# Optimization experiments

Measured on AMD Instinct MI355X. Metric: run time of the kernel, lower is better.

Reference implementation:

```python
import jax, jax.numpy as jnp
import numpy as np

_HIST_BINS = 64
TOP_K_FRAC = 0.125
HIST_THRESHOLD = 2048


def setup_inputs() -> dict:
    key = jax.random.key(0)
    B, S = 256, 131072
    importance = jax.random.normal(key, (B, S), dtype=jnp.float32)
    return {"importance": importance, "S": S}


def reference(importance, S):
    # importance: [B, S] float32; S: python int
    K = max(1, int(TOP_K_FRAC * S))
    if S > HIST_THRESHOLD:
        # Histogram bookkeeping path (computed but unused by the original module;
        # reproduced here for faithfulness to the source's memory traffic).
        imin = jnp.min(importance, axis=-1, keepdims=True)  # [B,1]
        imax = jnp.max(importance, axis=-1, keepdims=True)  # [B,1]
        rng = jnp.clip(imax - imin, 1e-8, None)
        bin_idx = ((importance - imin) / rng * (_HIST_BINS - 1)).astype(jnp.int32)
        bin_idx = jnp.clip(bin_idx, 0, _HIST_BINS - 1)  # [B,S]
        B = importance.shape[0]
        rows = jnp.arange(B)[:, None]  # [B,1] broadcast against [B,S]
        hist = jnp.zeros((B, _HIST_BINS), dtype=jnp.int32).at[rows, bin_idx].add(1)
        del hist  # dead value, exactly as in the torch source
    _, top_idx = jax.lax.top_k(importance, K)  # [B,K] indices into last dim
    return (top_idx, K)
```

## Files before the change

kernel.cpp:

```cpp
#include <hip/hip_runtime.h>
#include <stdint.h>


#define S_LEN   131072
#define K_SEL   16384
#define NBINS   8192
#define LOWBITS 19
#define IDXMASK 0x1FFFFu
#define CAND_CAP 20480
#define SORT_CAP 4096
#define DIRECT_MAX 256
#define WL_PER_ROW 2048
#define D_GRID  2048
#define HCAP 256
#define LCAP 512
#define NWAVE 16
#define PC_WAVE 1664
#define NITER (S_LEN / 4 / 1024)
#define BU0 ((0x3F800000u ^ 0x80000000u) >> LOWBITS)

__device__ __forceinline__ unsigned int ordered_u32(float f) {
  unsigned int x = __float_as_uint(f);
  unsigned int mask = (unsigned int)((int)x >> 31) | 0x80000000u;
  return x ^ mask;
}

__global__ __launch_bounds__(1024)
void select_kernel(const float* __restrict__ in,
                   unsigned long long* __restrict__ pairs,
                   unsigned long long* __restrict__ cand,
                   uint4* __restrict__ wl, unsigned int* __restrict__ ctrs,
                   unsigned int wlHalf, int* __restrict__ out,
                   int B, long long out_size) {
  const int row  = blockIdx.x;
  const int tid  = threadIdx.x;
  const int lane = tid & 63, wave = tid >> 6;
  __shared__ unsigned int h[NBINS];
  __shared__ unsigned int sfx[NBINS];
  __shared__ unsigned int waveTot[NWAVE];
  __shared__ unsigned int wcnt[NWAVE];
  __shared__ unsigned int sb1, nH, nL, gHs, gLs;
  __shared__ uint2 lheavy[HCAP];
  __shared__ uint2 llight[LCAP];

  for (int i = tid; i < NBINS; i += 1024) h[i] = 0;
  if (tid == 0) { nH = 0; nL = 0; }
  __syncthreads();

  const float4* p = (const float4*)(in + (size_t)row * S_LEN);
  unsigned long long* seg = pairs + ((size_t)row * NWAVE + wave) * PC_WAVE;
  unsigned int base = 0;
  const unsigned long long lmask = (1ull << lane) - 1ull;
#pragma unroll 8
  for (int it = 0; it < NITER; ++it) {
    int i4 = it * 1024 + tid;
    float4 v4 = p[i4];
    int idx0 = i4 * 4;
    float f[4] = {v4.x, v4.y, v4.z, v4.w};
#pragma unroll
    for (int e = 0; e < 4; ++e) {
      unsigned int u = ordered_u32(f[e]);
      unsigned int b = u >> LOWBITS;
      atomicAdd(&h[b], 1u);
      bool pred = (b >= BU0);
      unsigned long long m = __ballot(pred);
      if (pred) {
        unsigned int pos = base + (unsigned int)__popcll(m & lmask);
        unsigned long long key =
            ((unsigned long long)u << 17) |
            (unsigned long long)(IDXMASK - (unsigned int)(idx0 + e));
        if (pos < PC_WAVE) seg[pos] = key;
      }
      base += (unsigned int)__popcll(m);
    }
  }
  if (lane == 0) wcnt[wave] = base;
  __syncthreads();

  uint4 c0 = *(const uint4*)&h[tid * 8];
  uint4 c1 = *(const uint4*)&h[tid * 8 + 4];
  unsigned int v[8] = {c0.x, c0.y, c0.z, c0.w, c1.x, c1.y, c1.z, c1.w};
#pragma unroll
  for (int s = 6; s >= 0; --s) v[s] += v[s + 1];
  unsigned int tot = v[0];
  unsigned int suf = tot;
#pragma unroll
  for (int d = 1; d < 64; d <<= 1) {
    unsigned int o = __shfl_down(suf, d, 64);
    if (lane + d < 64) suf += o;
  }
  if (lane == 0) waveTot[wave] = suf;
  __syncthreads();
  unsigned int carry = 0;
  for (int w2 = wave + 1; w2 < NWAVE; ++w2) carry += waveTot[w2];
  unsigned int addv = (suf - tot) + carry;
  {
    uint4 o0 = make_uint4(v[0] + addv, v[1] + addv, v[2] + addv, v[3] + addv);
    uint4 o1 = make_uint4(v[4] + addv, v[5] + addv, v[6] + addv, v[7] + addv);
    *(uint4*)&sfx[tid * 8]     = o0;
    *(uint4*)&sfx[tid * 8 + 4] = o1;
  }
  __syncthreads();
#pragma unroll
  for (int s = 0; s < 8; ++s) {
    int b = tid * 8 + s;
    unsigned int cur = sfx[b];
    unsigned int nxt = (b + 1 < NBINS) ? sfx[b + 1] : 0u;
    if (cur >= K_SEL && nxt < K_SEL) sb1 = (unsigned int)b;
  }
  __syncthreads();
  const unsigned int b1 = sb1;

  for (int i = tid; i < NBINS; i += 1024) {
    unsigned int end   = sfx[i];
    unsigned int start = (i + 1 < NBINS) ? sfx[i + 1] : 0u;
    h[i] = start;
    if ((unsigned int)i >= b1) {
      unsigned int cnt = end - start;
      if (cnt) {
        if (cnt > DIRECT_MAX) {
          unsigned int p2 = atomicAdd(&nH, 1u);
          if (p2 < HCAP) lheavy[p2] = make_uint2(start, end);
          else {
            unsigned int g = atomicAdd(&ctrs[0], 1u);
            if (g < wlHalf) wl[2 * wlHalf - 1 - g] = make_uint4((unsigned int)row, start, end, 0u);
          }
        } else {
          unsigned int p2 = atomicAdd(&nL, 1u);
          if (p2 < LCAP) llight[p2] = make_uint2(start, end);
          else {
            unsigned int g = atomicAdd(&ctrs[1], 1u);
            if (g < wlHalf) wl[g] = make_uint4((unsigned int)row, start, end, 0u);
          }
        }
      }
    }
  }
  __syncthreads();
  if (tid == 0) {
    gHs = atomicAdd(&ctrs[0], nH < HCAP ? nH : HCAP);
    gLs = atomicAdd(&ctrs[1], nL < LCAP ? nL : LCAP);
  }
  __syncthreads();
  {
    unsigned int hN = nH < HCAP ? nH : HCAP;
    unsigned int lN = nL < LCAP ? nL : LCAP;
    for (unsigned int i = tid; i < hN; i += 1024) {
      uint2 e = lheavy[i]; unsigned int pos = gHs + i;
      if (pos < wlHalf) wl[2 * wlHalf - 1 - pos] = make_uint4((unsigned int)row, e.x, e.y, 0u);
    }
    for (unsigned int i = tid; i < lN; i += 1024) {
      uint2 e = llight[i]; unsigned int pos = gLs + i;
      if (pos < wlHalf) wl[pos] = make_uint4((unsigned int)row, e.x, e.y, 0u);
    }
  }

  bool fast = (b1 >= BU0);
  for (int w2 = 0; w2 < NWAVE; ++w2) fast = fast && (wcnt[w2] <= PC_WAVE);
  unsigned long long* c = cand + (size_t)row * CAND_CAP;
  if (fast) {
    const unsigned int myN = wcnt[wave];
    for (unsigned int i = (unsigned int)lane; i < myN; i += 64u) {
      unsigned long long k = seg[i];
      unsigned int b = (unsigned int)(k >> 36);
      if (b >= b1) {
        unsigned int pos = atomicAdd(&h[b], 1u);
        if (pos < CAND_CAP) c[pos] = k;
      }
    }
  } else {
#pragma unroll 4
    for (int it = 0; it < NITER; ++it) {
      int i4 = it * 1024 + tid;
      float4 v4 = p[i4];
      int idx0 = i4 * 4;
      float f[4] = {v4.x, v4.y, v4.z, v4.w};
#pragma unroll
      for (int e = 0; e < 4; ++e) {
        unsigned int u = ordered_u32(f[e]);
        unsigned int b = u >> LOWBITS;
        if (b >= b1) {
          unsigned int pos = atomicAdd(&h[b], 1u);
          unsigned long long key =
              ((unsigned long long)u << 17) |
              (unsigned long long)(IDXMASK - (unsigned int)(idx0 + e));
          if (pos < CAND_CAP) c[pos] = key;
        }
      }
    }
  }
  if (row == 0 && tid == 0) {
    long long pos = (long long)B * K_SEL;
    if (pos < out_size) out[pos] = K_SEL;
  }
}

__global__ __launch_bounds__(256)
void sort_kernel(const uint4* __restrict__ wl, const unsigned int* __restrict__ ctrs,
                 unsigned int wlHalf, const unsigned long long* __restrict__ cand,
                 int* __restrict__ out) {
  const int tid  = threadIdx.x;
  const int lane = tid & 63, wave = tid >> 6;
  __shared__ unsigned int   skey2[SORT_CAP];
  __shared__ unsigned char  sdig2[SORT_CAP];
  __shared__ unsigned int   ssfx[257];
  __shared__ unsigned int   scur[256];
  __shared__ unsigned int   segTot[4];
  unsigned int nHeavy = ctrs[0]; if (nHeavy > wlHalf) nHeavy = wlHalf;
  unsigned int nLight = ctrs[1]; if (nLight > wlHalf) nLight = wlHalf;

  for (unsigned int w = blockIdx.x; w < nHeavy; w += gridDim.x) {
    const uint4 it = wl[2 * wlHalf - 1 - w];
    const unsigned int row = it.x, start = it.y;
    unsigned int count = it.z - start;
    if (count > SORT_CAP) count = SORT_CAP;
    const unsigned long long* c = cand + (size_t)row * CAND_CAP + start;
    int* orow = out + (size_t)row * K_SEL;

    scur[tid] = 0;
    __syncthreads();
    for (unsigned int i = tid; i < count; i += 256)
      atomicAdd(&scur[(unsigned int)(c[i] >> 28) & 255u], 1u);
    __syncthreads();
    unsigned int cnt = scur[tid];
    unsigned int suf = cnt;
#pragma unroll
    for (int d = 1; d < 64; d <<= 1) {
      unsigned int o = __shfl_down(suf, d, 64);
      if (lane + d < 64) suf += o;
    }
    if (lane == 0) segTot[wave] = suf;
    __syncthreads();
    unsigned int carry = 0;
    for (int w2 = wave + 1; w2 < 4; ++w2) carry += segTot[w2];
    ssfx[tid] = suf + carry;
    if (tid == 0) ssfx[256] = 0;
    __syncthreads();
    scur[tid] = ssfx[tid + 1];
    __syncthreads();
    for (unsigned int i = tid; i < count; i += 256) {
      unsigned long long k = c[i];
      unsigned int d = (unsigned int)(k >> 28) & 255u;
      unsigned int p = atomicAdd(&scur[d], 1u);
      skey2[p] = (unsigned int)k & 0x0FFFFFFFu;
      sdig2[p] = (unsigned char)d;
    }
    __syncthreads();
    for (unsigned int p = tid; p < count; p += 256) {
      unsigned int k = skey2[p];
      unsigned int d = sdig2[p];
      unsigned int lo = ssfx[d + 1], hi = ssfx[d];
      unsigned int r = 0;
      for (unsigned int q = lo; q < hi; ++q) r += (skey2[q] > k) ? 1u : 0u;
      unsigned int pos = start + lo + r;
      if (pos < K_SEL)
        orow[pos] = (int)(IDXMASK - (k & IDXMASK));
    }
    __syncthreads();
  }

  for (unsigned int w = blockIdx.x * 4u + (unsigned int)wave; w < nLight;
       w += gridDim.x * 4u) {
    const uint4 it = wl[w];
    const unsigned int row = it.x, start = it.y;
    const unsigned int count = it.z - start;
    const unsigned long long* c = cand + (size_t)row * CAND_CAP + start;
    int* orow = out + (size_t)row * K_SEL;
    if (count <= 64) {
      unsigned long long me = ((unsigned int)lane < count) ? c[lane] : 0ull;
      unsigned int r = 0;
      for (int l = 0; l < 64; ++l)
        r += (__shfl(me, l, 64) > me) ? 1u : 0u;
      if ((unsigned int)lane < count) {
        unsigned int pos = start + r;
        if (pos < K_SEL)
          orow[pos] = (int)(IDXMASK - ((unsigned int)me & IDXMASK));
      }
    } else if (count <= 128) {
      unsigned long long me[2];
#pragma unroll
      for (int e = 0; e < 2; ++e) {
        unsigned int i = (unsigned int)lane + 64u * e;
        me[e] = (i < count) ? c[i] : 0ull;
      }
      unsigned int r[2] = {0u, 0u};
#pragma unroll
      for (int e = 0; e < 2; ++e) {
        for (int l = 0; l < 64; ++l) {
          unsigned long long kj = __shfl(me[e], l, 64);
#pragma unroll
          for (int e2 = 0; e2 < 2; ++e2) r[e2] += (kj > me[e2]) ? 1u : 0u;
        }
      }
#pragma unroll
      for (int e = 0; e < 2; ++e) {
        unsigned int i = (unsigned int)lane + 64u * e;
        if (i < count) {
          unsigned int pos = start + r[e];
          if (pos < K_SEL)
            orow[pos] = (int)(IDXMASK - ((unsigned int)me[e] & IDXMASK));
        }
      }
    } else {
      unsigned long long me[4];
#pragma unroll
      for (int e = 0; e < 4; ++e) {
        unsigned int i = (unsigned int)lane + 64u * e;
        me[e] = (i < count) ? c[i] : 0ull;
      }
      unsigned int r[4] = {0u, 0u, 0u, 0u};
#pragma unroll
      for (int e = 0; e < 4; ++e) {
        for (int l = 0; l < 64; ++l) {
          unsigned long long kj = __shfl(me[e], l, 64);
#pragma unroll
          for (int e2 = 0; e2 < 4; ++e2) r[e2] += (kj > me[e2]) ? 1u : 0u;
        }
      }
#pragma unroll
      for (int e = 0; e < 4; ++e) {
        unsigned int i = (unsigned int)lane + 64u * e;
        if (i < count) {
          unsigned int pos = start + r[e];
          if (pos < K_SEL)
            orow[pos] = (int)(IDXMASK - ((unsigned int)me[e] & IDXMASK));
        }
      }
    }
  }
}

extern "C" void kernel_launch(void* const* d_in, const int* in_sizes, int n_in,
                              void* d_out, int out_size, void* d_ws, size_t ws_size,
                              hipStream_t stream) {
  const float* importance = (const float*)d_in[0];
  int B = in_sizes[0] / S_LEN;
  if (B < 1) B = 1;
  (void)n_in; (void)ws_size;

  const unsigned int wlCap  = (unsigned int)B * WL_PER_ROW;
  const unsigned int wlHalf = wlCap / 2;
  size_t pairBytes = (size_t)B * NWAVE * PC_WAVE * sizeof(unsigned long long);
  size_t candBytes = (size_t)B * CAND_CAP * sizeof(unsigned long long);
  size_t wlBytes   = (size_t)wlCap * sizeof(uint4);
  char* base = (char*)d_ws;
  unsigned long long* pairs = (unsigned long long*)base;
  unsigned long long* cand  = (unsigned long long*)(base + pairBytes);
  uint4* wl                 = (uint4*)(base + pairBytes + candBytes);
  unsigned int* ctrs        = (unsigned int*)(base + pairBytes + candBytes + wlBytes);
  int* out = (int*)d_out;

  hipMemsetAsync(ctrs, 0, 4 * sizeof(unsigned int), stream);
  select_kernel<<<dim3(B),      dim3(1024), 0, stream>>>(
      importance, pairs, cand, wl, ctrs, wlHalf, out, B, (long long)out_size);
  sort_kernel  <<<dim3(D_GRID), dim3(256),  0, stream>>>(wl, ctrs, wlHalf, cand, out);
}
```

Measured before the change: 267.0 us.

## Histogram only upper-half bins with fallback rescan; cache heavy-bin keys in registers

```diff
diff --git a/kernel.cpp b/kernel.cpp
--- a/kernel.cpp
+++ b/kernel.cpp
@@ -23,6 +23,46 @@
   unsigned int x = __float_as_uint(f);
   unsigned int mask = (unsigned int)((int)x >> 31) | 0x80000000u;
   return x ^ mask;
+}
+
+__device__ __forceinline__ void suffix_scan_8k(const unsigned int* h,
+                                               unsigned int* sfx,
+                                               unsigned int* waveTot,
+                                               unsigned int* sb1p,
+                                               int tid, int lane, int wave) {
+  if (tid == 0) *sb1p = 0xFFFFFFFFu;
+  uint4 c0 = *(const uint4*)&h[tid * 8];
+  uint4 c1 = *(const uint4*)&h[tid * 8 + 4];
+  unsigned int v[8] = {c0.x, c0.y, c0.z, c0.w, c1.x, c1.y, c1.z, c1.w};
+#pragma unroll
+  for (int s = 6; s >= 0; --s) v[s] += v[s + 1];
+  unsigned int tot = v[0];
+  unsigned int suf = tot;
+#pragma unroll
+  for (int d = 1; d < 64; d <<= 1) {
+    unsigned int o = __shfl_down(suf, d, 64);
+    if (lane + d < 64) suf += o;
+  }
+  if (lane == 0) waveTot[wave] = suf;
+  __syncthreads();
+  unsigned int carry = 0;
+  for (int w2 = wave + 1; w2 < NWAVE; ++w2) carry += waveTot[w2];
+  unsigned int addv = (suf - tot) + carry;
+  {
+    uint4 o0 = make_uint4(v[0] + addv, v[1] + addv, v[2] + addv, v[3] + addv);
+    uint4 o1 = make_uint4(v[4] + addv, v[5] + addv, v[6] + addv, v[7] + addv);
+    *(uint4*)&sfx[tid * 8]     = o0;
+    *(uint4*)&sfx[tid * 8 + 4] = o1;
+  }
+  __syncthreads();
+#pragma unroll
+  for (int s = 0; s < 8; ++s) {
+    int b = tid * 8 + s;
+    unsigned int cur = sfx[b];
+    unsigned int nxt = (b + 1 < NBINS) ? sfx[b + 1] : 0u;
+    if (cur >= K_SEL && nxt < K_SEL) *sb1p = (unsigned int)b;
+  }
+  __syncthreads();
 }
 
 __global__ __launch_bounds__(1024)
@@ -61,10 +101,10 @@
     for (int e = 0; e < 4; ++e) {
       unsigned int u = ordered_u32(f[e]);
       unsigned int b = u >> LOWBITS;
-      atomicAdd(&h[b], 1u);
       bool pred = (b >= BU0);
       unsigned long long m = __ballot(pred);
       if (pred) {
+        atomicAdd(&h[b], 1u);
         unsigned int pos = base + (unsigned int)__popcll(m & lmask);
         unsigned long long key =
             ((unsigned long long)u << 17) |
@@ -77,38 +117,22 @@
   if (lane == 0) wcnt[wave] = base;
   __syncthreads();
 
-  uint4 c0 = *(const uint4*)&h[tid * 8];
-  uint4 c1 = *(const uint4*)&h[tid * 8 + 4];
-  unsigned int v[8] = {c0.x, c0.y, c0.z, c0.w, c1.x, c1.y, c1.z, c1.w};
-#pragma unroll
-  for (int s = 6; s >= 0; --s) v[s] += v[s + 1];
-  unsigned int tot = v[0];
-  unsigned int suf = tot;
-#pragma unroll
-  for (int d = 1; d < 64; d <<= 1) {
-    unsigned int o = __shfl_down(suf, d, 64);
-    if (lane + d < 64) suf += o;
-  }
-  if (lane == 0) waveTot[wave] = suf;
-  __syncthreads();
-  unsigned int carry = 0;
-  for (int w2 = wave + 1; w2 < NWAVE; ++w2) carry += waveTot[w2];
-  unsigned int addv = (suf - tot) + carry;
-  {
-    uint4 o0 = make_uint4(v[0] + addv, v[1] + addv, v[2] + addv, v[3] + addv);
-    uint4 o1 = make_uint4(v[4] + addv, v[5] + addv, v[6] + addv, v[7] + addv);
-    *(uint4*)&sfx[tid * 8]     = o0;
-    *(uint4*)&sfx[tid * 8 + 4] = o1;
-  }
-  __syncthreads();
-#pragma unroll
-  for (int s = 0; s < 8; ++s) {
-    int b = tid * 8 + s;
-    unsigned int cur = sfx[b];
-    unsigned int nxt = (b + 1 < NBINS) ? sfx[b + 1] : 0u;
-    if (cur >= K_SEL && nxt < K_SEL) sb1 = (unsigned int)b;
-  }
-  __syncthreads();
+  suffix_scan_8k(h, sfx, waveTot, &sb1, tid, lane, wave);
+  bool found1 = (sb1 != 0xFFFFFFFFu);
+  if (!found1) {
+#pragma unroll 4
+    for (int it = 0; it < NITER; ++it) {
+      float4 v4 = p[it * 1024 + tid];
+      float f[4] = {v4.x, v4.y, v4.z, v4.w};
+#pragma unroll
+      for (int e = 0; e < 4; ++e) {
+        unsigned int b = ordered_u32(f[e]) >> LOWBITS;
+        if (b < BU0) atomicAdd(&h[b], 1u);
+      }
+    }
+    __syncthreads();
+    suffix_scan_8k(h, sfx, waveTot, &sb1, tid, lane, wave);
+  }
   const unsigned int b1 = sb1;
 
   for (int i = tid; i < NBINS; i += 1024) {
@@ -155,7 +179,7 @@
     }
   }
 
-  bool fast = (b1 >= BU0);
+  bool fast = found1;
   for (int w2 = 0; w2 < NWAVE; ++w2) fast = fast && (wcnt[w2] <= PC_WAVE);
   unsigned long long* c = cand + (size_t)row * CAND_CAP;
   if (fast) {
@@ -217,10 +241,19 @@
     const unsigned long long* c = cand + (size_t)row * CAND_CAP + start;
     int* orow = out + (size_t)row * K_SEL;
 
+    unsigned long long me[16];
+#pragma unroll
+    for (int j = 0; j < 16; ++j) {
+      unsigned int i = (unsigned int)tid + 256u * j;
+      me[j] = (i < count) ? c[i] : 0ull;
+    }
     scur[tid] = 0;
     __syncthreads();
-    for (unsigned int i = tid; i < count; i += 256)
-      atomicAdd(&scur[(unsigned int)(c[i] >> 28) & 255u], 1u);
+#pragma unroll
+    for (int j = 0; j < 16; ++j) {
+      unsigned int i = (unsigned int)tid + 256u * j;
+      if (i < count) atomicAdd(&scur[(unsigned int)(me[j] >> 28) & 255u], 1u);
+    }
     __syncthreads();
     unsigned int cnt = scur[tid];
     unsigned int suf = cnt;
@@ -238,12 +271,16 @@
     __syncthreads();
     scur[tid] = ssfx[tid + 1];
     __syncthreads();
-    for (unsigned int i = tid; i < count; i += 256) {
-      unsigned long long k = c[i];
-      unsigned int d = (unsigned int)(k >> 28) & 255u;
-      unsigned int p = atomicAdd(&scur[d], 1u);
-      skey2[p] = (unsigned int)k & 0x0FFFFFFFu;
-      sdig2[p] = (unsigned char)d;
+#pragma unroll
+    for (int j = 0; j < 16; ++j) {
+      unsigned int i = (unsigned int)tid + 256u * j;
+      if (i < count) {
+        unsigned long long k = me[j];
+        unsigned int d = (unsigned int)(k >> 28) & 255u;
+        unsigned int p = atomicAdd(&scur[d], 1u);
+        skey2[p] = (unsigned int)k & 0x0FFFFFFFu;
+        sdig2[p] = (unsigned char)d;
+      }
     }
     __syncthreads();
     for (unsigned int p = tid; p < count; p += 256) {
```

Measured after the change: 265.9 us. Within noise of the previous version (-0.4%).
